# Optimization experiments

Hardware: AMD Instinct MI355X
Metric: run time of the kernel (lower is better)

The kernel has to match this reference:

```python
import jax, jax.numpy as jnp
import numpy as np

C = 256
G = min(C // 4, 32)  # GroupNorm groups = 32
EPS = 1e-6


def group_norm(x, gamma, beta):
    B, Cc, H, W = x.shape
    xg = x.reshape(B, G, Cc // G, H, W)
    mean = xg.mean(axis=(2, 3, 4), keepdims=True)
    var = xg.var(axis=(2, 3, 4), keepdims=True)
    xg = (xg - mean) / jnp.sqrt(var + EPS)
    x = xg.reshape(B, Cc, H, W)
    return x * gamma[None, :, None, None] + beta[None, :, None, None]


def nin(h, W_, b_):
    # 1x1 conv as channel contraction: [B,C,H,W] x [C,D] -> [B,D,H,W]
    return jnp.einsum('bchw,cd->bdhw', h, W_) + b_[None, :, None, None]


def setup_inputs() -> dict:
    key = jax.random.key(0)
    ks = jax.random.split(key, 12)
    B, H, Wd = 4, 64, 64
    x = jax.random.normal(ks[0], (B, C, H, Wd), dtype=jnp.float32)
    gn_gamma = jnp.ones((C,), jnp.float32)
    gn_beta = jnp.zeros((C,), jnp.float32)
    scale = 0.1
    w0 = jax.random.normal(ks[1], (C, C), jnp.float32) * scale
    b0 = jnp.zeros((C,), jnp.float32)
    w1 = jax.random.normal(ks[2], (C, C), jnp.float32) * scale
    b1 = jnp.zeros((C,), jnp.float32)
    w2 = jax.random.normal(ks[3], (C, C), jnp.float32) * scale
    b2 = jnp.zeros((C,), jnp.float32)
    w3 = jax.random.normal(ks[4], (C, C), jnp.float32) * scale
    b3 = jnp.zeros((C,), jnp.float32)
    return {"x": x, "gn_gamma": gn_gamma, "gn_beta": gn_beta,
            "w0": w0, "b0": b0, "w1": w1, "b1": b1,
            "w2": w2, "b2": b2, "w3": w3, "b3": b3}


def reference(x, gn_gamma, gn_beta, w0, b0, w1, b1, w2, b2, w3, b3):
    B, Cc, H, Wd = x.shape
    h = group_norm(x, gn_gamma, gn_beta)
    q = nin(h, w0, b0)
    k = nin(h, w1, b1)
    v = nin(h, w2, b2)
    # attention over all spatial positions; scores [B,H,W,H,W]
    w = jnp.einsum('bchw,bcij->bhwij', q, k) * (Cc ** -0.5)
    w = jax.nn.softmax(w.reshape(B, H, Wd, H * Wd), axis=-1)
    w = w.reshape(B, H, Wd, H, Wd)
    h = jnp.einsum('bhwij,bcij->bchw', w, v)
    h = nin(h, w3, b3)
    return x + h  # skip_rescale=False
```

## Files before the change

kernel.cpp:

```cpp
#include <hip/hip_runtime.h>
#include <math.h>


typedef short short8    __attribute__((ext_vector_type(8)));
typedef ushort ushort8  __attribute__((ext_vector_type(8)));
typedef float f32x4     __attribute__((ext_vector_type(4)));
typedef float f32x16    __attribute__((ext_vector_type(16)));

#define BB 4
#define CCH 256
#define NSP 4096
#define TEN ((size_t)BB * NSP * CCH)

__device__ __forceinline__ float b2f(ushort h){
  unsigned int u = ((unsigned int)h) << 16;
  float f; __builtin_memcpy(&f, &u, 4); return f;
}
__device__ __forceinline__ ushort f2b(float f){
  unsigned int u; __builtin_memcpy(&u, &f, 4);
  u += 0x7fffu + ((u >> 16) & 1u);
  return (ushort)(u >> 16);
}
__device__ __forceinline__ unsigned int pk2(float a, float b){
  unsigned int r;
  asm("v_cvt_pk_bf16_f32 %0, %1, %2" : "=&v"(r) : "v"(a), "v"(b));
  return r;
}

__global__ __launch_bounds__(256) void pre_k(const float* __restrict__ x,
                                             const float* __restrict__ w0,
                                             const float* __restrict__ w1,
                                             const float* __restrict__ w2,
                                             const float* __restrict__ w3,
                                             ushort* __restrict__ wT,
                                             float* __restrict__ sums){
  __shared__ ushort tile[64][72];
  __shared__ float red[8];
  const int bxx = blockIdx.x;
  const int t = threadIdx.x;
  if (bxx < 64){
    const int wsel = bxx >> 4, tb = bxx & 15;
    const float* w = (wsel==0) ? w0 : (wsel==1) ? w1 : (wsel==2) ? w2 : w3;
    ushort* dst = wT + (size_t)wsel * 65536;
    const int r0 = (tb >> 2) * 64, c0 = (tb & 3) * 64;
    #pragma unroll
    for (int p = 0; p < 2; p++){
      const int r = p*32 + (t >> 3), cc = (t & 7)*8;
      const float* wr = w + (size_t)(r0 + r)*256 + c0 + cc;
      f32x4 a = *(const f32x4*)wr;
      f32x4 d = *(const f32x4*)(wr + 4);
      #pragma unroll
      for (int j = 0; j < 4; j++){
        tile[r][cc + j]     = f2b(a[j]);
        tile[r][cc + 4 + j] = f2b(d[j]);
      }
    }
    __syncthreads();
    #pragma unroll
    for (int p = 0; p < 2; p++){
      const int r = p*32 + (t >> 3), cc = (t & 7)*8;
      ushort8 ov;
      #pragma unroll
      for (int j = 0; j < 8; j++) ov[j] = tile[cc + j][r];
      *(ushort8*)(dst + (size_t)(c0 + r)*256 + r0 + cc) = ov;
    }
  } else {
    const int q = bxx - 64;
    const f32x4* p = (const f32x4*)(x + (size_t)(q >> 1)*32768 + (size_t)(q & 1)*16384);
    float s = 0.f, s2 = 0.f;
    for (int i = t; i < 4096; i += 256){
      f32x4 v = p[i];
      #pragma unroll
      for (int j = 0; j < 4; j++){ s += v[j]; s2 += v[j]*v[j]; }
    }
    #pragma unroll
    for (int off = 32; off >= 1; off >>= 1){
      s  += __shfl_down(s,  off, 64);
      s2 += __shfl_down(s2, off, 64);
    }
    const int w = t >> 6;
    if ((t & 63) == 0){ red[w*2] = s; red[w*2+1] = s2; }
    __syncthreads();
    if (t == 0){
      sums[q*2]   = red[0]+red[2]+red[4]+red[6];
      sums[q*2+1] = red[1]+red[3]+red[5]+red[7];
    }
  }
}

__global__ __launch_bounds__(256) void gn_apply_k(const float* __restrict__ x,
                                                  const float* __restrict__ sums,
                                                  const float* __restrict__ gamma,
                                                  const float* __restrict__ beta,
                                                  ushort* __restrict__ h_t){
  __shared__ ushort tile[64][72];
  const int b = blockIdx.z, c0 = blockIdx.y*64, n0 = blockIdx.x*64;
  const int t = threadIdx.x;
  #pragma unroll
  for (int p = 0; p < 2; p++){
    const int cl = p*32 + (t >> 3);
    const int nc = (t & 7) * 8;
    const int c = c0 + cl;
    const int bg = b*32 + (c>>3);
    const float S  = sums[bg*4+0] + sums[bg*4+2];
    const float S2 = sums[bg*4+1] + sums[bg*4+3];
    const float mean = S * (1.f/32768.f);
    const float rstd = rsqrtf(fmaxf(S2*(1.f/32768.f) - mean*mean, 0.f) + 1e-6f);
    const float sc = rstd * gamma[c];
    const float sh = beta[c] - mean * sc;
    const float* xr = x + ((size_t)b*CCH + c)*NSP + n0 + nc;
    f32x4 a = *(const f32x4*)xr;
    f32x4 d = *(const f32x4*)(xr + 4);
    #pragma unroll
    for (int j = 0; j < 4; j++){
      tile[nc + j][cl]     = f2b(a[j]*sc + sh);
      tile[nc + 4 + j][cl] = f2b(d[j]*sc + sh);
    }
  }
  __syncthreads();
  #pragma unroll
  for (int p = 0; p < 2; p++){
    const int nl = p*32 + (t >> 3);
    const int cc = (t & 7) * 8;
    ushort8 ov;
    #pragma unroll
    for (int j = 0; j < 8; j++) ov[j] = tile[nl][cc + j];
    *(ushort8*)(h_t + ((size_t)b*NSP + n0 + nl)*CCH + c0 + cc) = ov;
  }
}

__global__ __launch_bounds__(256) void gemm_qkv_k(const ushort* __restrict__ wT,
                                                  const ushort* __restrict__ h_t,
                                                  ushort* __restrict__ q_t,
                                                  ushort* __restrict__ k_t,
                                                  ushort* __restrict__ vout,
                                                  const float* __restrict__ b0,
                                                  const float* __restrict__ b1,
                                                  const float* __restrict__ b2){
  __shared__ ushort Bt[64*256];
  const int K = 256;
  const long HS = (long)NSP * CCH;
  const int z = blockIdx.z;
  const ushort* A; const ushort* Bm; ushort* OutT;
  int M; long aStride, bStride, oStride;
  const float* biasM; const float* biasN;
  if (z == 0){      A=wT;          Bm=h_t;        OutT=q_t;  M=256;  aStride=0;  bStride=HS; oStride=HS; biasM=b0;      biasN=nullptr; }
  else if (z == 1){ A=wT+65536;    Bm=h_t;        OutT=k_t;  M=256;  aStride=0;  bStride=HS; oStride=HS; biasM=b1;      biasN=nullptr; }
  else {            A=h_t;         Bm=wT+2*65536; OutT=vout; M=4096; aStride=HS; bStride=0;  oStride=HS; biasM=nullptr; biasN=b2; }

  const int t = threadIdx.x, w = t >> 6, lane = t & 63;
  const int li = lane & 15, quad = lane >> 4;
  const int m64 = M >> 6;
  const int tm = blockIdx.x % m64, tn = blockIdx.x / m64;
  const int batch = blockIdx.y;
  A    += (size_t)batch * aStride;
  Bm   += (size_t)batch * bStride;
  OutT += (size_t)batch * oStride;
  const int m0 = tm*64 + w*16;
  const int nb = tn*64;

  #pragma unroll
  for (int i = 0; i < 8; i++){
    const int id = t + 256*i;
    const int row = id >> 5, gg = id & 31;
    *(ushort8*)&Bt[row*256 + (gg ^ (row & 31))*8] =
      *(const ushort8*)(Bm + (size_t)(nb + row)*K + gg*8);
  }
  short8 afr[8];
  #pragma unroll
  for (int kk = 0; kk < 8; kk++)
    afr[kk] = *(const short8*)(A + (size_t)(m0 + li)*K + kk*32 + quad*8);
  __syncthreads();

  #pragma unroll
  for (int nt = 0; nt < 4; nt++){
    f32x4 acc = {0.f,0.f,0.f,0.f};
    const int n = nb + nt*16 + li;
    const int rowl = nt*16 + li;
    #pragma unroll
    for (int kk = 0; kk < 8; kk++){
      short8 bfr = *(const short8*)&Bt[rowl*256 + ((4*kk + quad) ^ (rowl & 31))*8];
      acc = __builtin_amdgcn_mfma_f32_16x16x32_bf16(afr[kk], bfr, acc, 0, 0, 0);
    }
    const float bn = biasN ? biasN[n] : 0.f;
    float e[4];
    #pragma unroll
    for (int r2 = 0; r2 < 4; r2++){
      const float bm = biasM ? biasM[m0 + quad*4 + r2] : 0.f;
      e[r2] = acc[r2] + bm + bn;
    }
    uint2 dv; dv.x = pk2(e[0], e[1]); dv.y = pk2(e[2], e[3]);
    *(uint2*)(OutT + (size_t)n*M + m0 + quad*4) = dv;
  }
}

__global__ __launch_bounds__(256, 2) void attn32_k(const ushort* __restrict__ qg,
                                                   const ushort* __restrict__ kg,
                                                   const ushort* __restrict__ vg,
                                                   ushort* __restrict__ ph01,
                                                   ushort* __restrict__ ph23,
                                                   float* __restrict__ lbuf,
                                                   int iters, int ks4){
  __shared__ ushort Kt[32*260];
  __shared__ ushort Vt[256*36];

  const int t = threadIdx.x, lane = t & 63;
  const int cl = lane & 31, h = lane >> 5;
  const int bx = blockIdx.x;
  const int qt = bx / ks4;
  const int r  = bx % ks4;
  const int s  = r >> 2, b = r & 3;
  const int n0 = qt * 128;
  const int w = t >> 6;
  const int qb = n0 + w*32;
  const int keybase = s * (iters * 32);

  const ushort* kb = kg + (size_t)b*NSP*CCH;
  const ushort* vb = vg + (size_t)b*CCH*NSP;

  short8 qf[16];
  {
    const ushort* qrow = qg + ((size_t)b*NSP + qb + cl)*CCH + h*8;
    #pragma unroll
    for (int st = 0; st < 16; st++) qf[st] = *(const short8*)(qrow + st*16);
  }

  f32x16 oacc[8];
  #pragma unroll
  for (int i = 0; i < 8; i++) oacc[i] = (f32x16)(0.f);
  float l_i = 0.f;
  const float c1 = 0.0625f * 1.44269504088896f;
  const float M2 = 24.f;

  ushort8 kreg[4];
  #pragma unroll
  for (int i = 0; i < 4; i++){
    const int id = t + 256*i;
    kreg[i] = *(const ushort8*)(kb + (size_t)(keybase + (id>>5))*CCH + (id&31)*8);
  }

  for (int it = 0; it < iters; it++){
    const int key0 = keybase + it*32;
    __syncthreads();
    ushort8 vreg[4];
    #pragma unroll
    for (int i = 0; i < 4; i++){
      const int id = t + 256*i;
      vreg[i] = *(const ushort8*)(vb + (size_t)(id>>2)*NSP + key0 + (id&3)*8);
    }
    #pragma unroll
    for (int i = 0; i < 4; i++){
      const int id = t + 256*i;
      *(ushort8*)&Kt[(id>>5)*260 + (id&31)*8] = kreg[i];
    }
    #pragma unroll
    for (int i = 0; i < 4; i++){
      const int id = t + 256*i;
      *(ushort8*)&Vt[(id>>2)*36 + (id&3)*8] = vreg[i];
    }
    __syncthreads();

    if (it + 1 < iters){
      const int nk0 = key0 + 32;
      #pragma unroll
      for (int i = 0; i < 4; i++){
        const int id = t + 256*i;
        kreg[i] = *(const ushort8*)(kb + (size_t)(nk0 + (id>>5))*CCH + (id&31)*8);
      }
    }

    f32x16 sacc = (f32x16)(0.f);
    #pragma unroll
    for (int st = 0; st < 16; st++){
      short8 kf = *(const short8*)&Kt[cl*260 + st*16 + h*8];
      sacc = __builtin_amdgcn_mfma_f32_32x32x16_bf16(kf, qf[st], sacc, 0, 0, 0);
    }

    unsigned int grp[4][2];
    #pragma unroll
    for (int m = 0; m < 4; m++){
      float p0 = __builtin_amdgcn_exp2f(fminf(sacc[4*m+0]*c1 - M2, 30.f));
      float p1 = __builtin_amdgcn_exp2f(fminf(sacc[4*m+1]*c1 - M2, 30.f));
      float p2 = __builtin_amdgcn_exp2f(fminf(sacc[4*m+2]*c1 - M2, 30.f));
      float p3 = __builtin_amdgcn_exp2f(fminf(sacc[4*m+3]*c1 - M2, 30.f));
      l_i += (p0 + p1) + (p2 + p3);
      grp[m][0] = pk2(p0, p1);
      grp[m][1] = pk2(p2, p3);
    }
    unsigned int sa0 = h ? grp[0][0] : grp[1][0];
    unsigned int sa1 = h ? grp[0][1] : grp[1][1];
    unsigned int sb0 = h ? grp[2][0] : grp[3][0];
    unsigned int sb1 = h ? grp[2][1] : grp[3][1];
    unsigned int ra0 = __shfl_xor((int)sa0, 32, 64);
    unsigned int ra1 = __shfl_xor((int)sa1, 32, 64);
    unsigned int rb0 = __shfl_xor((int)sb0, 32, 64);
    unsigned int rb1 = __shfl_xor((int)sb1, 32, 64);
    unsigned int f0[4], f1[4];
    if (h == 0){
      f0[0]=grp[0][0]; f0[1]=grp[0][1]; f0[2]=ra0; f0[3]=ra1;
      f1[0]=grp[2][0]; f1[1]=grp[2][1]; f1[2]=rb0; f1[3]=rb1;
    } else {
      f0[0]=ra0; f0[1]=ra1; f0[2]=grp[1][0]; f0[3]=grp[1][1];
      f1[0]=rb0; f1[1]=rb1; f1[2]=grp[3][0]; f1[3]=grp[3][1];
    }
    short8 pf0, pf1;
    __builtin_memcpy(&pf0, f0, 16);
    __builtin_memcpy(&pf1, f1, 16);

    #pragma unroll
    for (int ct = 0; ct < 8; ct++){
      short8 v0 = *(const short8*)&Vt[(ct*32 + cl)*36 + h*8];
      short8 v1 = *(const short8*)&Vt[(ct*32 + cl)*36 + 16 + h*8];
      oacc[ct] = __builtin_amdgcn_mfma_f32_32x32x16_bf16(pf0, v0, oacc[ct], 0, 0, 0);
      oacc[ct] = __builtin_amdgcn_mfma_f32_32x32x16_bf16(pf1, v1, oacc[ct], 0, 0, 0);
    }
  }

  ushort* ps = (s < 2) ? (ph01 + (size_t)s*TEN) : (ph23 + (size_t)(s-2)*TEN);
  ps += (size_t)b * NSP * CCH;
  #pragma unroll
  for (int ct = 0; ct < 8; ct++){
    const size_t crow = (size_t)(ct*32 + cl) * NSP;
    #pragma unroll
    for (int m = 0; m < 4; m++){
      unsigned int d0 = pk2(oacc[ct][4*m+0], oacc[ct][4*m+1]);
      unsigned int d1 = pk2(oacc[ct][4*m+2], oacc[ct][4*m+3]);
      uint2 dv; dv.x = d0; dv.y = d1;
      *(uint2*)(ps + crow + qb + 8*m + 4*h) = dv;
    }
  }
  l_i += __shfl_xor(l_i, 32, 64);
  if (h == 0)
    lbuf[(size_t)s*BB*NSP + (size_t)b*NSP + qb + cl] = l_i;
}

__global__ __launch_bounds__(256) void combine_k(const ushort* __restrict__ ph01,
                                                 const ushort* __restrict__ ph23,
                                                 const float* __restrict__ lbuf,
                                                 ushort* __restrict__ Oc, int ks){
  __shared__ ushort T[64*66];
  const int t = threadIdx.x;
  const int q0 = blockIdx.x * 64, c0 = blockIdx.y * 64, b = blockIdx.z;
  const int ql = t & 63, cs = t >> 6;
  float suml = 0.f;
  for (int sp = 0; sp < ks; sp++) suml += lbuf[(size_t)sp*BB*NSP + (size_t)b*NSP + q0 + ql];
  const float rl = 1.f / suml;
  #pragma unroll
  for (int ci = 0; ci < 16; ci++){
    const int c = cs*16 + ci;
    float acc = 0.f;
    for (int sp = 0; sp < ks; sp++){
      const ushort* pp = (sp < 2) ? (ph01 + (size_t)sp*TEN) : (ph23 + (size_t)(sp-2)*TEN);
      acc += b2f(pp[((size_t)b*CCH + c0 + c)*NSP + q0 + ql]);
    }
    T[ql*66 + c] = f2b(acc * rl);
  }
  __syncthreads();
  const int q2 = t >> 2, ch = (t & 3) * 16;
  ushort8 o0, o1;
  #pragma unroll
  for (int j = 0; j < 8; j++){ o0[j] = T[q2*66 + ch + j]; o1[j] = T[q2*66 + ch + 8 + j]; }
  ushort* dst = Oc + ((size_t)b*NSP + q0 + q2)*CCH + c0 + ch;
  *(ushort8*)dst = o0;
  *(ushort8*)(dst + 8) = o1;
}

__global__ __launch_bounds__(256) void gemm_proj_k(const ushort* __restrict__ A,
                                                   const ushort* __restrict__ Bm,
                                                   const float* __restrict__ b3,
                                                   const float* __restrict__ xin,
                                                   float* __restrict__ out){
  __shared__ ushort Bt[64*256];
  const int K = 256;
  const int t = threadIdx.x, w = t >> 6, lane = t & 63;
  const int li = lane & 15, quad = lane >> 4;
  const int tm = blockIdx.x & 63, tn = blockIdx.x >> 6;
  const int batch = blockIdx.y;
  A   += (size_t)batch * NSP * CCH;
  xin += (size_t)batch * CCH * NSP;
  out += (size_t)batch * CCH * NSP;
  const int m0 = tm*64 + w*16;
  const int nb = tn*64;

  #pragma unroll
  for (int i = 0; i < 8; i++){
    const int id = t + 256*i;
    const int row = id >> 5, gg = id & 31;
    *(ushort8*)&Bt[row*256 + (gg ^ (row & 31))*8] =
      *(const ushort8*)(Bm + (size_t)(nb + row)*K + gg*8);
  }
  short8 afr[8];
  #pragma unroll
  for (int kk = 0; kk < 8; kk++)
    afr[kk] = *(const short8*)(A + (size_t)(m0 + li)*K + kk*32 + quad*8);
  __syncthreads();

  #pragma unroll
  for (int nt = 0; nt < 4; nt++){
    f32x4 acc = {0.f,0.f,0.f,0.f};
    const int d = nb + nt*16 + li;
    const int rowl = nt*16 + li;
    #pragma unroll
    for (int kk = 0; kk < 8; kk++){
      short8 bfr = *(const short8*)&Bt[rowl*256 + ((4*kk + quad) ^ (rowl & 31))*8];
      acc = __builtin_amdgcn_mfma_f32_16x16x32_bf16(afr[kk], bfr, acc, 0, 0, 0);
    }
    const float bias = b3[d];
    const size_t idx = (size_t)d*NSP + m0 + quad*4;
    f32x4 xv = *(const f32x4*)(xin + idx);
    f32x4 ov;
    #pragma unroll
    for (int r = 0; r < 4; r++) ov[r] = acc[r] + bias + xv[r];
    *(f32x4*)(out + idx) = ov;
  }
}

extern "C" void kernel_launch(void* const* d_in, const int* in_sizes, int n_in,
                              void* d_out, int out_size, void* d_ws, size_t ws_size,
                              hipStream_t stream){
  const float* x     = (const float*)d_in[0];
  const float* gamma = (const float*)d_in[1];
  const float* beta  = (const float*)d_in[2];
  const float* w0    = (const float*)d_in[3];
  const float* b0    = (const float*)d_in[4];
  const float* w1    = (const float*)d_in[5];
  const float* b1    = (const float*)d_in[6];
  const float* w2    = (const float*)d_in[7];
  const float* b2    = (const float*)d_in[8];
  const float* w3    = (const float*)d_in[9];
  const float* b3    = (const float*)d_in[10];
  float* out = (float*)d_out;

  ushort* h_t  = (ushort*)d_out;
  ushort* ph01 = (ushort*)d_out;
  ushort* q_t = (ushort*)d_ws;
  ushort* k_t = q_t + TEN;
  ushort* v   = k_t + TEN;
  ushort* wT  = v + TEN;
  float* sums  = (float*)(wT + 4*65536);
  float* lbuf  = sums + 512;
  ushort* ph23 = (ushort*)(lbuf + 4*BB*NSP);

  const size_t need4 = ((3*TEN + 4*65536)*2) + (512 + 4*BB*NSP)*4 + 2*TEN*2;
  const int ks = (ws_size >= need4) ? 4 : 2;
  const int iters = NSP / (ks * 32);

  pre_k<<<dim3(320), 256, 0, stream>>>(x, w0, w1, w2, w3, wT, sums);
  gn_apply_k<<<dim3(64,4,4), 256, 0, stream>>>(x, sums, gamma, beta, h_t);
  gemm_qkv_k<<<dim3(256, BB, 3), 256, 0, stream>>>(wT, h_t, q_t, k_t, v, b0, b1, b2);

  attn32_k<<<128*ks, 256, 0, stream>>>(q_t, k_t, v, ph01, ph23, lbuf, iters, 4*ks);

  ushort* Oc = k_t;
  combine_k<<<dim3(64, 4, BB), 256, 0, stream>>>(ph01, ph23, lbuf, Oc, ks);
  gemm_proj_k<<<dim3(256, BB), 256, 0, stream>>>(Oc, wT + 3*65536, b3, x, out);
}
```

Before: 254.9 us.

## Double-buffer K/V tiles in attention with direct global-to-LDS loads for K

The attention kernel now keeps two LDS buffers each for K and V. The next K tile is loaded with global_load_lds DMA into an XOR-swizzled, unpadded layout, and the next V tile is staged through registers while the current tile is computed. This cuts the per-iteration barriers from two to one and removes the register round-trip for K. In exchange it doubles LDS use, and the loop now assumes an even iteration count.

Measured after the change: 420.4 us. 64.9% more time.

```diff
diff --git a/kernel.cpp b/kernel.cpp
--- a/kernel.cpp
+++ b/kernel.cpp
@@ -25,6 +25,11 @@
   unsigned int r;
   asm("v_cvt_pk_bf16_f32 %0, %1, %2" : "=&v"(r) : "v"(a), "v"(b));
   return r;
+}
+__device__ __forceinline__ void dma16(const void* g, void* l){
+  __builtin_amdgcn_global_load_lds((const __attribute__((address_space(1))) void*)g,
+                                   (__attribute__((address_space(3))) void*)l,
+                                   16, 0, 0);
 }
 
 __global__ __launch_bounds__(256) void pre_k(const float* __restrict__ x,
@@ -194,6 +199,79 @@
   }
 }
 
+#define ATTN_STEP(KC, KN, VC, VN, IT)                                           \
+  {                                                                             \
+    const int it_ = (IT);                                                       \
+    const bool more_ = (it_ + 1 < iters);                                       \
+    ushort8 vreg_[4];                                                           \
+    if (more_){                                                                 \
+      const int nk0_ = keybase + (it_ + 1)*32;                                  \
+      _Pragma("unroll")                                                         \
+      for (int j = 0; j < 4; j++){                                              \
+        const int id_ = (w*4 + j)*64 + lane;                                    \
+        const int row_ = id_ >> 5, e_ = id_ & 31;                               \
+        dma16(kb + (size_t)(nk0_ + row_)*CCH + ((e_ ^ row_)*8),                 \
+              &(KN)[(w*4 + j)*512]);                                            \
+      }                                                                         \
+      _Pragma("unroll")                                                         \
+      for (int i = 0; i < 4; i++){                                              \
+        const int id_ = t + 256*i;                                              \
+        vreg_[i] = *(const ushort8*)(vb + (size_t)(id_>>2)*NSP + nk0_ + (id_&3)*8); \
+      }                                                                         \
+    }                                                                           \
+    f32x16 sacc = (f32x16)(0.f);                                                \
+    _Pragma("unroll")                                                           \
+    for (int st = 0; st < 16; st++){                                            \
+      short8 kf = *(const short8*)&(KC)[cl*256 + ((((st<<1)|h)) ^ cl)*8];       \
+      sacc = __builtin_amdgcn_mfma_f32_32x32x16_bf16(kf, qf[st], sacc, 0, 0, 0);\
+    }                                                                           \
+    unsigned int grp[4][2];                                                     \
+    _Pragma("unroll")                                                           \
+    for (int m = 0; m < 4; m++){                                                \
+      float p0 = __builtin_amdgcn_exp2f(fminf(sacc[4*m+0]*c1 - M2, 30.f));      \
+      float p1 = __builtin_amdgcn_exp2f(fminf(sacc[4*m+1]*c1 - M2, 30.f));      \
+      float p2 = __builtin_amdgcn_exp2f(fminf(sacc[4*m+2]*c1 - M2, 30.f));      \
+      float p3 = __builtin_amdgcn_exp2f(fminf(sacc[4*m+3]*c1 - M2, 30.f));      \
+      l_i += (p0 + p1) + (p2 + p3);                                             \
+      grp[m][0] = pk2(p0, p1);                                                  \
+      grp[m][1] = pk2(p2, p3);                                                  \
+    }                                                                           \
+    unsigned int sa0 = h ? grp[0][0] : grp[1][0];                               \
+    unsigned int sa1 = h ? grp[0][1] : grp[1][1];                               \
+    unsigned int sb0 = h ? grp[2][0] : grp[3][0];                               \
+    unsigned int sb1 = h ? grp[2][1] : grp[3][1];                               \
+    unsigned int ra0 = __shfl_xor((int)sa0, 32, 64);                            \
+    unsigned int ra1 = __shfl_xor((int)sa1, 32, 64);                            \
+    unsigned int rb0 = __shfl_xor((int)sb0, 32, 64);                            \
+    unsigned int rb1 = __shfl_xor((int)sb1, 32, 64);                            \
+    unsigned int f0[4], f1[4];                                                  \
+    if (h == 0){                                                                \
+      f0[0]=grp[0][0]; f0[1]=grp[0][1]; f0[2]=ra0; f0[3]=ra1;                   \
+      f1[0]=grp[2][0]; f1[1]=grp[2][1]; f1[2]=rb0; f1[3]=rb1;                   \
+    } else {                                                                    \
+      f0[0]=ra0; f0[1]=ra1; f0[2]=grp[1][0]; f0[3]=grp[1][1];                   \
+      f1[0]=rb0; f1[1]=rb1; f1[2]=grp[3][0]; f1[3]=grp[3][1];                   \
+    }                                                                           \
+    short8 pf0, pf1;                                                            \
+    __builtin_memcpy(&pf0, f0, 16);                                             \
+    __builtin_memcpy(&pf1, f1, 16);                                             \
+    if (more_){                                                                 \
+      _Pragma("unroll")                                                         \
+      for (int i = 0; i < 4; i++){                                              \
+        const int id_ = t + 256*i;                                              \
+        *(ushort8*)&(VN)[(id_>>2)*36 + (id_&3)*8] = vreg_[i];                   \
+      }                                                                         \
+    }                                                                           \
+    _Pragma("unroll")                                                           \
+    for (int ct = 0; ct < 8; ct++){                                             \
+      short8 v0 = *(const short8*)&(VC)[(ct*32 + cl)*36 + h*8];                 \
+      short8 v1 = *(const short8*)&(VC)[(ct*32 + cl)*36 + 16 + h*8];            \
+      oacc[ct] = __builtin_amdgcn_mfma_f32_32x32x16_bf16(pf0, v0, oacc[ct], 0, 0, 0); \
+      oacc[ct] = __builtin_amdgcn_mfma_f32_32x32x16_bf16(pf1, v1, oacc[ct], 0, 0, 0); \
+    }                                                                           \
+    if (more_) __syncthreads();                                                 \
+  }
+
 __global__ __launch_bounds__(256, 2) void attn32_k(const ushort* __restrict__ qg,
                                                    const ushort* __restrict__ kg,
                                                    const ushort* __restrict__ vg,
@@ -201,8 +279,8 @@
                                                    ushort* __restrict__ ph23,
                                                    float* __restrict__ lbuf,
                                                    int iters, int ks4){
-  __shared__ ushort Kt[32*260];
-  __shared__ ushort Vt[256*36];
+  __shared__ ushort KtA[32*256], KtB[32*256];
+  __shared__ ushort VtA[256*36], VtB[256*36];
 
   const int t = threadIdx.x, lane = t & 63;
   const int cl = lane & 31, h = lane >> 5;
@@ -232,88 +310,30 @@
   const float c1 = 0.0625f * 1.44269504088896f;
   const float M2 = 24.f;
 
-  ushort8 kreg[4];
-  #pragma unroll
-  for (int i = 0; i < 4; i++){
-    const int id = t + 256*i;
-    kreg[i] = *(const ushort8*)(kb + (size_t)(keybase + (id>>5))*CCH + (id&31)*8);
-  }
-
-  for (int it = 0; it < iters; it++){
-    const int key0 = keybase + it*32;
-    __syncthreads();
-    ushort8 vreg[4];
+  #pragma unroll
+  for (int j = 0; j < 4; j++){
+    const int id = (w*4 + j)*64 + lane;
+    const int row = id >> 5, e = id & 31;
+    dma16(kb + (size_t)(keybase + row)*CCH + ((e ^ row)*8), &KtA[(w*4 + j)*512]);
+  }
+  {
+    ushort8 v0r[4];
     #pragma unroll
     for (int i = 0; i < 4; i++){
       const int id = t + 256*i;
-      vreg[i] = *(const ushort8*)(vb + (size_t)(id>>2)*NSP + key0 + (id&3)*8);
+      v0r[i] = *(const ushort8*)(vb + (size_t)(id>>2)*NSP + keybase + (id&3)*8);
     }
     #pragma unroll
     for (int i = 0; i < 4; i++){
       const int id = t + 256*i;
-      *(ushort8*)&Kt[(id>>5)*260 + (id&31)*8] = kreg[i];
-    }
-    #pragma unroll
-    for (int i = 0; i < 4; i++){
-      const int id = t + 256*i;
-      *(ushort8*)&Vt[(id>>2)*36 + (id&3)*8] = vreg[i];
-    }
-    __syncthreads();
-
-    if (it + 1 < iters){
-      const int nk0 = key0 + 32;
-      #pragma unroll
-      for (int i = 0; i < 4; i++){
-        const int id = t + 256*i;
-        kreg[i] = *(const ushort8*)(kb + (size_t)(nk0 + (id>>5))*CCH + (id&31)*8);
-      }
-    }
-
-    f32x16 sacc = (f32x16)(0.f);
-    #pragma unroll
-    for (int st = 0; st < 16; st++){
-      short8 kf = *(const short8*)&Kt[cl*260 + st*16 + h*8];
-      sacc = __builtin_amdgcn_mfma_f32_32x32x16_bf16(kf, qf[st], sacc, 0, 0, 0);
-    }
-
-    unsigned int grp[4][2];
-    #pragma unroll
-    for (int m = 0; m < 4; m++){
-      float p0 = __builtin_amdgcn_exp2f(fminf(sacc[4*m+0]*c1 - M2, 30.f));
-      float p1 = __builtin_amdgcn_exp2f(fminf(sacc[4*m+1]*c1 - M2, 30.f));
-      float p2 = __builtin_amdgcn_exp2f(fminf(sacc[4*m+2]*c1 - M2, 30.f));
-      float p3 = __builtin_amdgcn_exp2f(fminf(sacc[4*m+3]*c1 - M2, 30.f));
-      l_i += (p0 + p1) + (p2 + p3);
-      grp[m][0] = pk2(p0, p1);
-      grp[m][1] = pk2(p2, p3);
-    }
-    unsigned int sa0 = h ? grp[0][0] : grp[1][0];
-    unsigned int sa1 = h ? grp[0][1] : grp[1][1];
-    unsigned int sb0 = h ? grp[2][0] : grp[3][0];
-    unsigned int sb1 = h ? grp[2][1] : grp[3][1];
-    unsigned int ra0 = __shfl_xor((int)sa0, 32, 64);
-    unsigned int ra1 = __shfl_xor((int)sa1, 32, 64);
-    unsigned int rb0 = __shfl_xor((int)sb0, 32, 64);
-    unsigned int rb1 = __shfl_xor((int)sb1, 32, 64);
-    unsigned int f0[4], f1[4];
-    if (h == 0){
-      f0[0]=grp[0][0]; f0[1]=grp[0][1]; f0[2]=ra0; f0[3]=ra1;
-      f1[0]=grp[2][0]; f1[1]=grp[2][1]; f1[2]=rb0; f1[3]=rb1;
-    } else {
-      f0[0]=ra0; f0[1]=ra1; f0[2]=grp[1][0]; f0[3]=grp[1][1];
-      f1[0]=rb0; f1[1]=rb1; f1[2]=grp[3][0]; f1[3]=grp[3][1];
-    }
-    short8 pf0, pf1;
-    __builtin_memcpy(&pf0, f0, 16);
-    __builtin_memcpy(&pf1, f1, 16);
-
-    #pragma unroll
-    for (int ct = 0; ct < 8; ct++){
-      short8 v0 = *(const short8*)&Vt[(ct*32 + cl)*36 + h*8];
-      short8 v1 = *(const short8*)&Vt[(ct*32 + cl)*36 + 16 + h*8];
-      oacc[ct] = __builtin_amdgcn_mfma_f32_32x32x16_bf16(pf0, v0, oacc[ct], 0, 0, 0);
-      oacc[ct] = __builtin_amdgcn_mfma_f32_32x32x16_bf16(pf1, v1, oacc[ct], 0, 0, 0);
-    }
+      *(ushort8*)&VtA[(id>>2)*36 + (id&3)*8] = v0r[i];
+    }
+  }
+  __syncthreads();
+
+  for (int it = 0; it < iters; it += 2){
+    ATTN_STEP(KtA, KtB, VtA, VtB, it);
+    ATTN_STEP(KtB, KtA, VtB, VtA, it + 1);
   }
 
   ushort* ps = (s < 2) ? (ph01 + (size_t)s*TEN) : (ph23 + (size_t)(s-2)*TEN);
```
